# Kernel optimization log

Hardware: AMD Instinct MI355X
Metric: run time of the kernel (lower is better)

The kernel has to match this reference:

```python
import jax, jax.numpy as jnp
import numpy as np

N_NODES = 50000
N_EDGES = 800000
IN_DIM = 128
HIDDEN_DIM = 128


def setup_inputs() -> dict:
    key = jax.random.key(0)
    k1, k2, k3, k4 = jax.random.split(key, 4)
    x = jax.random.normal(k1, (N_NODES, IN_DIM), dtype=jnp.float32)
    edge_index = jax.random.randint(k2, (2, N_EDGES), 0, N_NODES, dtype=jnp.int64)
    # Glorot-ish init for weights
    W1 = jax.random.normal(k3, (IN_DIM, HIDDEN_DIM), dtype=jnp.float32) / np.sqrt(IN_DIM)
    b1 = jnp.zeros((HIDDEN_DIM,), dtype=jnp.float32)
    W2 = jax.random.normal(k4, (HIDDEN_DIM, 2), dtype=jnp.float32) / np.sqrt(HIDDEN_DIM)
    b2 = jnp.zeros((2,), dtype=jnp.float32)
    return {"x": x, "edge_index": edge_index, "W1": W1, "b1": b1, "W2": W2, "b2": b2}


def _gcn_norm(edge_index, n_nodes):
    """Add self-loops and compute symmetric GCN normalization per edge."""
    loops = jnp.arange(n_nodes, dtype=edge_index.dtype)
    src = jnp.concatenate([edge_index[0], loops])  # [E + N]
    dst = jnp.concatenate([edge_index[1], loops])  # [E + N]
    ones = jnp.ones_like(dst, dtype=jnp.float32)
    deg = jax.ops.segment_sum(ones, dst, num_segments=n_nodes)  # [N]
    dinv = jnp.where(deg > 0, jax.lax.rsqrt(deg), 0.0)
    norm = dinv[src] * dinv[dst]  # [E + N]
    return src, dst, norm


def _gcn_conv(x, W, b, src, dst, norm, n_nodes):
    h = x @ W                                   # [N, out]
    msg = h[src] * norm[:, None]                # [E+N, out] gather + scale
    agg = jax.ops.segment_sum(msg, dst, num_segments=n_nodes)  # scatter-add
    return agg + b


def reference(x, edge_index, W1, b1, W2, b2):
    n = x.shape[0]
    src, dst, norm = _gcn_norm(edge_index, n)
    h = jax.nn.relu(_gcn_conv(x, W1, b1, src, dst, norm, n))
    out = _gcn_conv(h, W2, b2, src, dst, norm, n)
    return jax.nn.log_softmax(out, axis=1)
```

## Files before the change

### kernel.cpp

```cpp
#include <hip/hip_runtime.h>
#include <hip/hip_fp16.h>


#define DIM 128
#define ELLW 32
#define EPC 4

typedef _Float16 f16x8 __attribute__((ext_vector_type(8)));
typedef float f32x4 __attribute__((ext_vector_type(4)));

__device__ __forceinline__ int detect_is64(const int* __restrict__ ei, int e) {
    __shared__ int sflag;
    int t = threadIdx.x;
    int hv = (t < 32 && (2 * t + 1) < 2 * e) ? ei[2 * t + 1] : 0;
    unsigned long long nz = __ballot(hv != 0);
    if (t == 0) sflag = (nz == 0ULL) ? 1 : 0;
    __syncthreads();
    return sflag;
}

__device__ __forceinline__ int load_idx(const int* ei, long long pos, int is64) {
    if (is64) return (int)((const long long*)ei)[pos];
    return ei[pos];
}

__global__ void count_ell_kernel(const int* __restrict__ ei, int* __restrict__ counts,
                                 int* __restrict__ col_ell, int2* __restrict__ spill,
                                 int n, int e) {
    int is64 = detect_is64(ei, e);
    int cls = blockIdx.x & 7;
    long long chunk = blockIdx.x >> 3;
    long long base = chunk * (256 * EPC) + threadIdx.x;
#pragma unroll
    for (int k = 0; k < EPC; ++k) {
        long long i = base + (long long)k * 256;
        if (i < e) {
            int d = load_idx(ei, (long long)e + i, is64);
            if (((d >> 4) & 7) == cls) {
                int s = load_idx(ei, i, is64);
                int tk = atomicAdd(&counts[d], 1);
                if (tk < ELLW) {
                    col_ell[(size_t)d * ELLW + tk] = s;
                } else {
                    int p = atomicAdd(&counts[n], 1);
                    spill[p] = make_int2(s, d);
                }
            }
        }
    }
}

__global__ void w1prep_kernel(const float* __restrict__ W1, __half* __restrict__ W1T) {
    __shared__ __half wtile[32 * 136];
    int t = threadIdx.x;
    int c0 = blockIdx.x * 32;
    for (int it = 0; it < 16; ++it) {
        int k = it * 8 + (t >> 5);
        int c = t & 31;
        wtile[c * 136 + k] = __float2half(W1[(size_t)k * DIM + c0 + c]);
    }
    __syncthreads();
#pragma unroll
    for (int it = 0; it < 2; ++it) {
        int c = t >> 3;
        int kc = (t & 7) + it * 8;
        *(float4*)((char*)(W1T + (size_t)(c0 + c) * DIM) + kc * 16) =
            *(float4*)((char*)(wtile + c * 136) + kc * 16);
    }
}

#define GR 128
__global__ __launch_bounds__(256) void gemm1_kernel(
        const float* __restrict__ x, const __half* __restrict__ W1T,
        const int* __restrict__ counts, __half* __restrict__ g1, int n) {
    __shared__ short xs[GR * DIM];
    __shared__ short wt[DIM * DIM];
    int t = threadIdx.x;
    int row0 = blockIdx.x * GR;

#pragma unroll
    for (int i = 0; i < 8; ++i) {
        int f = t + i * 256;
        int col = f >> 4, kc = f & 15;
        unsigned int byte = (unsigned)(col * 256 + kc * 16);
        byte ^= (unsigned)((col & 7) << 4);
        *(float4*)((char*)wt + byte) = *(const float4*)((const char*)W1T + (size_t)f * 16);
    }
#pragma unroll
    for (int i = 0; i < 16; ++i) {
        int f = t + i * 256;
        int r = f >> 5, c4 = f & 31;
        float4 v = make_float4(0.f, 0.f, 0.f, 0.f);
        if (row0 + r < n)
            v = *(const float4*)(x + (size_t)(row0 + r) * DIM + c4 * 4);
        __half2 p01 = __floats2half2_rn(v.x, v.y);
        __half2 p23 = __floats2half2_rn(v.z, v.w);
        float2 pk;
        ((__half2*)&pk)[0] = p01;
        ((__half2*)&pk)[1] = p23;
        unsigned int byte = (unsigned)(r * 256 + c4 * 8);
        byte ^= (unsigned)((r & 7) << 4);
        *(float2*)((char*)xs + byte) = pk;
    }
    __syncthreads();

    int w  = t >> 6;
    int l  = t & 63;
    int lr = l & 15;
    int lg = l >> 4;

    f32x4 acc[2][8];
#pragma unroll
    for (int m = 0; m < 2; ++m)
#pragma unroll
        for (int cf = 0; cf < 8; ++cf) acc[m][cf] = (f32x4){0.f, 0.f, 0.f, 0.f};

#pragma unroll
    for (int kt = 0; kt < 4; ++kt) {
        int kByte = kt * 64 + lg * 16;
        f16x8 a[2];
#pragma unroll
        for (int m = 0; m < 2; ++m) {
            int row = w * 32 + m * 16 + lr;
            unsigned int byte = (unsigned)(row * 256 + kByte);
            byte ^= (unsigned)((row & 7) << 4);
            a[m] = *(const f16x8*)((const char*)xs + byte);
        }
#pragma unroll
        for (int cf = 0; cf < 8; ++cf) {
            int col = cf * 16 + lr;
            unsigned int byte = (unsigned)(col * 256 + kByte);
            byte ^= (unsigned)((col & 7) << 4);
            f16x8 b = *(const f16x8*)((const char*)wt + byte);
            acc[0][cf] = __builtin_amdgcn_mfma_f32_16x16x32_f16(a[0], b, acc[0][cf], 0, 0, 0);
            acc[1][cf] = __builtin_amdgcn_mfma_f32_16x16x32_f16(a[1], b, acc[1][cf], 0, 0, 0);
        }
    }

#pragma unroll
    for (int m = 0; m < 2; ++m)
#pragma unroll
        for (int r4 = 0; r4 < 4; ++r4) {
            int row = row0 + w * 32 + m * 16 + lg * 4 + r4;
            if (row < n) {
                float dv = rsqrtf((float)(counts[row] + 1));
#pragma unroll
                for (int cf = 0; cf < 8; ++cf) {
                    int col = cf * 16 + lr;
                    g1[(size_t)row * DIM + col] = __float2half(acc[m][cf][r4] * dv);
                }
            }
        }
}

__global__ void agg1_kernel(const __half* __restrict__ g1, const int* __restrict__ counts,
                            const int* __restrict__ col_ell, const int2* __restrict__ spill,
                            const float* __restrict__ b1, const float* __restrict__ W2,
                            float* __restrict__ g2, int n) {
    int lane = threadIdx.x & 63;
    int wid  = threadIdx.x >> 6;
    int d = blockIdx.x * 4 + wid;
    if (d >= n) return;
    int deg = __builtin_amdgcn_readfirstlane(counts[d]);
    float dv = rsqrtf((float)(deg + 1));
    const __half2* base = (const __half2*)g1 + lane;
    int m = deg < ELLW ? deg : ELLW;
    const int* row = col_ell + (size_t)d * ELLW;

    int idx[ELLW];
#pragma unroll
    for (int k = 0; k < ELLW; ++k) {
        int s = __builtin_amdgcn_readfirstlane(row[k]);
        idx[k] = (k < m) ? s : n;
    }
    __half2 h[ELLW];
#pragma unroll
    for (int k = 0; k < ELLW; ++k)
        h[k] = base[(size_t)idx[k] * 64];
    float2 vf = __half22float2(base[(size_t)d * 64]);
    float a0 = vf.x, a1 = vf.y, c0 = 0.f, c1 = 0.f;
#pragma unroll
    for (int k = 0; k < ELLW; k += 2) {
        float2 u = __half22float2(h[k]);
        float2 v = __half22float2(h[k + 1]);
        a0 += u.x; a1 += u.y;
        c0 += v.x; c1 += v.y;
    }
    float acc0 = a0 + c0, acc1 = a1 + c1;

    int sc = __builtin_amdgcn_readfirstlane(counts[n]);
    if (sc > 0) {
        for (int i = 0; i < sc; ++i) {
            int2 sp = spill[i];
            if (sp.y == d) {
                float2 u = __half22float2(base[(size_t)sp.x * 64]);
                acc0 += u.x; acc1 += u.y;
            }
        }
    }
    int f0 = lane * 2, f1 = f0 + 1;
    float h0 = fmaxf(dv * acc0 + b1[f0], 0.f);
    float h1 = fmaxf(dv * acc1 + b1[f1], 0.f);
    float z0 = fmaf(h1, W2[f1 * 2 + 0], h0 * W2[f0 * 2 + 0]);
    float z1 = fmaf(h1, W2[f1 * 2 + 1], h0 * W2[f0 * 2 + 1]);
#pragma unroll
    for (int off = 32; off > 0; off >>= 1) {
        z0 += __shfl_down(z0, off);
        z1 += __shfl_down(z1, off);
    }
    if (lane == 0) {
        g2[d * 2 + 0] = dv * z0;
        g2[d * 2 + 1] = dv * z1;
    }
}

__global__ void agg2_kernel(const float* __restrict__ g2, const int* __restrict__ counts,
                            const int* __restrict__ col_ell, const int2* __restrict__ spill,
                            const float* __restrict__ b2, float* __restrict__ out, int n) {
    int t = threadIdx.x;
    int sub = t & 15;
    int d = blockIdx.x * 16 + (t >> 4);
    if (d >= n) return;
    int deg = counts[d];
    int m = deg < ELLW ? deg : ELLW;
    const int* row = col_ell + (size_t)d * ELLW;
    float a0 = 0.f, a1 = 0.f;
    const float2* g2v = (const float2*)g2;
    for (int j = sub; j < m; j += 16) {
        float2 v = g2v[row[j]];
        a0 += v.x; a1 += v.y;
    }
    int sc = counts[n];
    if (sc > 0 && sub == 0) {
        for (int i = 0; i < sc; ++i) {
            int2 sp = spill[i];
            if (sp.y == d) { float2 v = g2v[sp.x]; a0 += v.x; a1 += v.y; }
        }
    }
#pragma unroll
    for (int off = 8; off > 0; off >>= 1) {
        a0 += __shfl_down(a0, off, 16);
        a1 += __shfl_down(a1, off, 16);
    }
    if (sub == 0) {
        float2 self = g2v[d];
        float dv = rsqrtf((float)(deg + 1));
        float z0 = dv * (a0 + self.x) + b2[0];
        float z1 = dv * (a1 + self.y) + b2[1];
        float mm = fmaxf(z0, z1);
        float l = mm + logf(expf(z0 - mm) + expf(z1 - mm));
        out[d * 2 + 0] = z0 - l;
        out[d * 2 + 1] = z1 - l;
    }
}

extern "C" void kernel_launch(void* const* d_in, const int* in_sizes, int n_in,
                              void* d_out, int out_size, void* d_ws, size_t ws_size,
                              hipStream_t stream) {
    const float* x  = (const float*)d_in[0];
    const int*   ei = (const int*)d_in[1];
    const float* W1 = (const float*)d_in[2];
    const float* b1 = (const float*)d_in[3];
    const float* W2 = (const float*)d_in[4];
    const float* b2 = (const float*)d_in[5];
    float* out = (float*)d_out;

    int n = in_sizes[0] / DIM;
    int e = in_sizes[1] / 2;

    char* wsp = (char*)d_ws;
    size_t used = 0;
    auto alloc = [&](size_t bytes) {
        char* p = wsp + used;
        used += (bytes + 255) & ~(size_t)255;
        return p;
    };
    int*    counts  = (int*)alloc((size_t)(n + 64) * 4);
    int*    col_ell = (int*)alloc((size_t)n * ELLW * 4);
    int2*   spill   = (int2*)alloc((size_t)e * 8);
    __half* g1      = (__half*)alloc((size_t)(n + 1) * DIM * 2);
    float*  g2      = (float*)alloc((size_t)n * 2 * 4);
    __half* W1T     = (__half*)alloc((size_t)DIM * DIM * 2);

    hipMemsetAsync(counts, 0, (size_t)(n + 64) * 4, stream);
    hipMemsetAsync(g1 + (size_t)n * DIM, 0, DIM * 2, stream);
    w1prep_kernel<<<4, 256, 0, stream>>>(W1, W1T);
    long long nchunk = ((long long)e + 256 * EPC - 1) / (256 * EPC);
    count_ell_kernel<<<(unsigned)(nchunk * 8), 256, 0, stream>>>(ei, counts, col_ell, spill, n, e);
    gemm1_kernel<<<(n + GR - 1) / GR, 256, 0, stream>>>(x, W1T, counts, g1, n);
    agg1_kernel<<<(n + 3) / 4, 256, 0, stream>>>(g1, counts, col_ell, spill, b1, W2, g2, n);
    agg2_kernel<<<(n + 15) / 16, 256, 0, stream>>>(g2, counts, col_ell, spill, b2, out, n);
}
```

Measured before the change: 110.0 us.

## Fuse memsets into prep kernel and remap aggregation blocks by node class

Two memsets and the W1 transpose kernel are merged into one prep kernel that also zeroes counts and the pad row of g1, cutting the number of launches. Block indices in agg1 and agg2 are remapped so consecutive blocks interleave eight node classes, matching the (d>>4)&7 partitioning used when building the ELL table. The intent is to spread destination nodes so that each XCD (likely eight on this part) reads the col_ell rows that the same block index wrote in the count pass, improving L2 locality. It adds extra index arithmetic and some padded blocks that exit early.

```diff
diff --git a/kernel.cpp b/kernel.cpp
--- a/kernel.cpp
+++ b/kernel.cpp
@@ -22,6 +22,47 @@
 __device__ __forceinline__ int load_idx(const int* ei, long long pos, int is64) {
     if (is64) return (int)((const long long*)ei)[pos];
     return ei[pos];
+}
+
+__device__ __forceinline__ int class_count(int n, int cls) {
+    int B = n >> 7, r = n & 127;
+    int extra = r - cls * 16;
+    extra = extra < 0 ? 0 : (extra > 16 ? 16 : extra);
+    return B * 16 + extra;
+}
+__device__ __forceinline__ int class_node(int cls, int j) {
+    return ((j >> 4) << 7) + cls * 16 + (j & 15);
+}
+
+__global__ void prep_kernel(const float* __restrict__ W1, __half* __restrict__ W1T,
+                            int* __restrict__ counts, __half* __restrict__ g1zero, int n) {
+    __shared__ __half wtile[32 * 136];
+    int b = blockIdx.x;
+    int t = threadIdx.x;
+    if (b < 4) {
+        int c0 = b * 32;
+        for (int it = 0; it < 16; ++it) {
+            int k = it * 8 + (t >> 5);
+            int c = t & 31;
+            wtile[c * 136 + k] = __float2half(W1[(size_t)k * DIM + c0 + c]);
+        }
+        __syncthreads();
+#pragma unroll
+        for (int it = 0; it < 2; ++it) {
+            int c = t >> 3;
+            int kc = (t & 7) + it * 8;
+            *(float4*)((char*)(W1T + (size_t)(c0 + c) * DIM) + kc * 16) =
+                *(float4*)((char*)(wtile + c * 136) + kc * 16);
+        }
+    } else {
+        int zb = b - 4;
+        int total = n + 64;
+        int per = (total + 31) / 32;
+        int beg = zb * per;
+        int end = beg + per; if (end > total) end = total;
+        for (int i = beg + t; i < end; i += 256) counts[i] = 0;
+        if (zb == 0 && t < 64) ((int*)g1zero)[t] = 0;
+    }
 }
 
 __global__ void count_ell_kernel(const int* __restrict__ ei, int* __restrict__ counts,
@@ -50,25 +91,6 @@
     }
 }
 
-__global__ void w1prep_kernel(const float* __restrict__ W1, __half* __restrict__ W1T) {
-    __shared__ __half wtile[32 * 136];
-    int t = threadIdx.x;
-    int c0 = blockIdx.x * 32;
-    for (int it = 0; it < 16; ++it) {
-        int k = it * 8 + (t >> 5);
-        int c = t & 31;
-        wtile[c * 136 + k] = __float2half(W1[(size_t)k * DIM + c0 + c]);
-    }
-    __syncthreads();
-#pragma unroll
-    for (int it = 0; it < 2; ++it) {
-        int c = t >> 3;
-        int kc = (t & 7) + it * 8;
-        *(float4*)((char*)(W1T + (size_t)(c0 + c) * DIM) + kc * 16) =
-            *(float4*)((char*)(wtile + c * 136) + kc * 16);
-    }
-}
-
 #define GR 128
 __global__ __launch_bounds__(256) void gemm1_kernel(
         const float* __restrict__ x, const __half* __restrict__ W1T,
@@ -159,8 +181,11 @@
                             float* __restrict__ g2, int n) {
     int lane = threadIdx.x & 63;
     int wid  = threadIdx.x >> 6;
-    int d = blockIdx.x * 4 + wid;
-    if (d >= n) return;
+    int cls  = blockIdx.x & 7;
+    int q    = blockIdx.x >> 3;
+    int j    = q * 4 + wid;
+    if (j >= class_count(n, cls)) return;
+    int d = class_node(cls, j);
     int deg = __builtin_amdgcn_readfirstlane(counts[d]);
     float dv = rsqrtf((float)(deg + 1));
     const __half2* base = (const __half2*)g1 + lane;
@@ -219,15 +244,18 @@
                             const float* __restrict__ b2, float* __restrict__ out, int n) {
     int t = threadIdx.x;
     int sub = t & 15;
-    int d = blockIdx.x * 16 + (t >> 4);
-    if (d >= n) return;
+    int cls = blockIdx.x & 7;
+    int q   = blockIdx.x >> 3;
+    int j   = q * 16 + (t >> 4);
+    if (j >= class_count(n, cls)) return;
+    int d = class_node(cls, j);
     int deg = counts[d];
     int m = deg < ELLW ? deg : ELLW;
     const int* row = col_ell + (size_t)d * ELLW;
     float a0 = 0.f, a1 = 0.f;
     const float2* g2v = (const float2*)g2;
-    for (int j = sub; j < m; j += 16) {
-        float2 v = g2v[row[j]];
+    for (int jj = sub; jj < m; jj += 16) {
+        float2 v = g2v[row[jj]];
         a0 += v.x; a1 += v.y;
     }
     int sc = counts[n];
@@ -282,12 +310,15 @@
     float*  g2      = (float*)alloc((size_t)n * 2 * 4);
     __half* W1T     = (__half*)alloc((size_t)DIM * DIM * 2);
 
-    hipMemsetAsync(counts, 0, (size_t)(n + 64) * 4, stream);
-    hipMemsetAsync(g1 + (size_t)n * DIM, 0, DIM * 2, stream);
-    w1prep_kernel<<<4, 256, 0, stream>>>(W1, W1T);
+    prep_kernel<<<36, 256, 0, stream>>>(W1, W1T, counts, g1 + (size_t)n * DIM, n);
     long long nchunk = ((long long)e + 256 * EPC - 1) / (256 * EPC);
     count_ell_kernel<<<(unsigned)(nchunk * 8), 256, 0, stream>>>(ei, counts, col_ell, spill, n, e);
     gemm1_kernel<<<(n + GR - 1) / GR, 256, 0, stream>>>(x, W1T, counts, g1, n);
-    agg1_kernel<<<(n + 3) / 4, 256, 0, stream>>>(g1, counts, col_ell, spill, b1, W2, g2, n);
-    agg2_kernel<<<(n + 15) / 16, 256, 0, stream>>>(g2, counts, col_ell, spill, b2, out, n);
-}
+
+    int B = n >> 7, r = n & 127;
+    int nclsmax = B * 16 + (r < 16 ? r : 16);
+    int agg1_blocks = 8 * ((nclsmax + 3) / 4);
+    int agg2_blocks = 8 * ((nclsmax + 15) / 16);
+    agg1_kernel<<<agg1_blocks, 256, 0, stream>>>(g1, counts, col_ell, spill, b1, W2, g2, n);
+    agg2_kernel<<<agg2_blocks, 256, 0, stream>>>(g2, counts, col_ell, spill, b2, out, n);
+}
```

Measured after the change: 105.4 us. 4.2% less time.
